# Performance work log

Measured on AMD Instinct MI355X. Metric: run time of the kernel, lower is better.

## Reference

```python
import jax, jax.numpy as jnp
import numpy as np

EPS = 1e-3  # keras BatchNormalization default epsilon


def _dwconv_t(y, w):
    # depthwise conv along time (axis 1), SAME padding. y:(B,T,S,G,n), w:(G,n,k)
    k = w.shape[-1]
    T = y.shape[1]
    pl = (k - 1) // 2
    yp = jnp.pad(y, ((0, 0), (pl, k - 1 - pl), (0, 0), (0, 0), (0, 0)))
    return sum(yp[:, j:j + T] * w[..., j] for j in range(k))


def _tc_layer(x, w, b, k3, k5, k7, gamma, beta, mu, var):
    # x:(B,T,S,C); w:(5,G,Cg,nb); b/gamma/beta/mu/var:(5,G,nb); k*:(G,nb,k)
    B, T, S, C = x.shape
    G, nb = w.shape[1], w.shape[-1]
    # global spatial pooling: concat [x, max, mean] along spatial axis -> S+2
    x = jnp.concatenate([x, x.max(axis=2, keepdims=True), x.mean(axis=2, keepdims=True)], axis=2)
    S = S + 2
    xg = x.reshape(B, T, S, G, C // G)
    # 5 grouped 1x1x1 pointwise convs at once
    y = jnp.einsum('btsgc,pgcn->pbtsgn', xg, w) + b[:, None, None, None]
    t0 = y[0]
    t3 = _dwconv_t(y[1], k3)
    t5 = _dwconv_t(y[2], k5)
    t7 = _dwconv_t(y[3], k7)
    # temporal maxpool pool=2 stride=1 SAME (TF pads right)
    t1 = jnp.maximum(y[4], jnp.concatenate([y[4][:, 1:], y[4][:, -1:]], axis=1))
    ts = jnp.stack([t0, t3, t5, t7, t1])  # (5,B,T,S,G,nb)
    scale = gamma[:, None, None, None] / jnp.sqrt(var[:, None, None, None] + EPS)
    ts = (ts - mu[:, None, None, None]) * scale + beta[:, None, None, None]
    # concat branches within each group: (B,T,S,G,5*nb)
    z = jnp.transpose(ts, (1, 2, 3, 4, 0, 5)).reshape(B, T, S, G, 5 * nb)
    z = jax.nn.relu(z)
    # channel shuffle: (G, per) -> (per, G) -> flatten
    z = jnp.swapaxes(z, -1, -2).reshape(B, T, S, G * 5 * nb)
    # MaxPooling3D pool=(2,1,1) stride 2 valid: halve T
    return jnp.maximum(z[:, 0::2], z[:, 1::2])


def setup_inputs() -> dict:
    key = jax.random.key(0)
    ks = jax.random.split(key, 32)
    B, T, H, W, C = 16, 64, 7, 7, 1024
    G = 8
    d = {'x': jax.random.normal(ks[0], (B, T, H, W, C), jnp.float32)}
    specs = [(0, 128, 32), (1, 160, 40)]  # (layer, Cg, nb)
    i = 1
    for l, cg, nb in specs:
        d[f'w{l}'] = 0.02 * jax.random.normal(ks[i], (5, G, cg, nb)); i += 1
        d[f'b{l}'] = 0.02 * jax.random.normal(ks[i], (5, G, nb)); i += 1
        d[f'k3_{l}'] = 0.1 * jax.random.normal(ks[i], (G, nb, 3)); i += 1
        d[f'k5_{l}'] = 0.1 * jax.random.normal(ks[i], (G, nb, 5)); i += 1
        d[f'k7_{l}'] = 0.1 * jax.random.normal(ks[i], (G, nb, 7)); i += 1
        d[f'g{l}'] = jax.random.uniform(ks[i], (5, G, nb), minval=0.5, maxval=1.5); i += 1
        d[f'be{l}'] = 0.02 * jax.random.normal(ks[i], (5, G, nb)); i += 1
        d[f'mu{l}'] = 0.02 * jax.random.normal(ks[i], (5, G, nb)); i += 1
        d[f'v{l}'] = jax.random.uniform(ks[i], (5, G, nb), minval=0.5, maxval=1.5); i += 1
    return d


def reference(x, w0, b0, k3_0, k5_0, k7_0, g0, be0, mu0, v0,
              w1, b1, k3_1, k5_1, k7_1, g1, be1, mu1, v1):
    B, T, H, W, C = x.shape
    z = x.reshape(B, T, H * W, C)  # (B,T,S,C), side_dim2=1 kept implicit
    z = _tc_layer(z, w0, b0, k3_0, k5_0, k7_0, g0, be0, mu0, v0)
    z = _tc_layer(z, w1, b1, k3_1, k5_1, k7_1, g1, be1, mu1, v1)
    return z[:, :, :, None, :]  # (B, T/4, S+4, 1, Cout)
```

## Files before the change

### kernel.cpp

```cpp
#include <hip/hip_runtime.h>
#include <hip/hip_bf16.h>

#define EPSBN 1e-3f

typedef __attribute__((ext_vector_type(8))) short bf16x8;
typedef __attribute__((ext_vector_type(8))) unsigned short ushort8;
typedef __attribute__((ext_vector_type(4))) float f32x4;


__device__ __forceinline__ float bf2f(unsigned short u) {
    union { unsigned int i; float f; } c; c.i = (unsigned int)u << 16; return c.f;
}
__device__ __forceinline__ unsigned short f2bf(float f) {
    union { float f; unsigned int i; } c; c.f = f;
    unsigned int r = c.i + 0x7FFF + ((c.i >> 16) & 1);
    return (unsigned short)(r >> 16);
}

__global__ __launch_bounds__(256) void tc_prep(const float* __restrict__ w0,
                                               const float* __restrict__ w1,
                                               unsigned short* __restrict__ W0t,
                                               unsigned short* __restrict__ W1t) {
    const int idx = blockIdx.x * 256 + threadIdx.x;
    if (idx < 163840) {
        const int g   = idx / 20480;
        const int rem = idx - g*20480;
        const int n   = rem >> 7;
        const int k   = rem & 127;
        const int p   = n >> 5, nn = n & 31;
        W0t[idx] = f2bf(w0[(((size_t)p*8 + g)*128 + k)*32 + nn]);
    } else if (idx < 163840 + 256000) {
        const int i2  = idx - 163840;
        const int g   = i2 / 32000;
        const int rem = i2 - g*32000;
        const int n   = rem / 160;
        const int k   = rem - n*160;
        const int kref = (k % 20)*8 + k/20;
        const int p   = n / 40, nn = n - p*40;
        W1t[i2] = f2bf(w1[(((size_t)p*8 + g)*160 + kref)*40 + nn]);
    }
}

__global__ __launch_bounds__(256) void tc_reduce0(const float* __restrict__ x,
                                                  unsigned short* __restrict__ xb,
                                                  unsigned short* __restrict__ extb,
                                                  const int big) {
    const int bt = blockIdx.x;
    const int b  = bt >> 6, t = bt & 63;
    const int c  = threadIdx.x * 4;
    const float4* src = reinterpret_cast<const float4*>(x + (size_t)bt * 49 * 1024 + c);
    float4 v = src[0];
    float mx0 = v.x, mx1 = v.y, mx2 = v.z, mx3 = v.w;
    float sm0 = v.x, sm1 = v.y, sm2 = v.z, sm3 = v.w;
    if (big) {
        ushort4 o; o.x=f2bf(v.x); o.y=f2bf(v.y); o.z=f2bf(v.z); o.w=f2bf(v.w);
        *reinterpret_cast<ushort4*>(&xb[((size_t)(b*51)*64 + t)*1024 + c]) = o;
    }
    for (int s = 1; s < 49; ++s) {
        float4 u = src[(size_t)s * 256];
        mx0 = fmaxf(mx0, u.x); sm0 += u.x;
        mx1 = fmaxf(mx1, u.y); sm1 += u.y;
        mx2 = fmaxf(mx2, u.z); sm2 += u.z;
        mx3 = fmaxf(mx3, u.w); sm3 += u.w;
        if (big) {
            ushort4 o; o.x=f2bf(u.x); o.y=f2bf(u.y); o.z=f2bf(u.z); o.w=f2bf(u.w);
            *reinterpret_cast<ushort4*>(&xb[((size_t)(b*51 + s)*64 + t)*1024 + c]) = o;
        }
    }
    const float inv = 1.0f / 49.0f;
    ushort4 omx, omn;
    omx.x=f2bf(mx0); omx.y=f2bf(mx1); omx.z=f2bf(mx2); omx.w=f2bf(mx3);
    omn.x=f2bf(sm0*inv); omn.y=f2bf(sm1*inv); omn.z=f2bf(sm2*inv); omn.w=f2bf(sm3*inv);
    if (big) {
        *reinterpret_cast<ushort4*>(&xb[((size_t)(b*51 + 49)*64 + t)*1024 + c]) = omx;
        *reinterpret_cast<ushort4*>(&xb[((size_t)(b*51 + 50)*64 + t)*1024 + c]) = omn;
    } else {
        *reinterpret_cast<ushort4*>(&extb[((size_t)(b*2 + 0)*64 + t)*1024 + c]) = omx;
        *reinterpret_cast<ushort4*>(&extb[((size_t)(b*2 + 1)*64 + t)*1024 + c]) = omn;
    }
}

template<int BIG>
__global__ __launch_bounds__(256, 5) void tc_layer0(
    const float* __restrict__ x, const unsigned short* __restrict__ xb,
    const unsigned short* __restrict__ extb,
    const unsigned short* __restrict__ W0t, const float* __restrict__ bias,
    const float* __restrict__ k3, const float* __restrict__ k5,
    const float* __restrict__ k7,
    const float* __restrict__ gam, const float* __restrict__ bet,
    const float* __restrict__ mu, const float* __restrict__ var,
    unsigned short* __restrict__ zb)
{
    const int tid = threadIdx.x;
    const int g  = blockIdx.x / 816;
    const int bs = blockIdx.x % 816;
    const int s  = bs % 51;
    const int b  = bs / 51;

    __shared__ __align__(16) unsigned short lds[15104];
    unsigned short* AtU = lds;
    unsigned short* WtU = lds + 64*136;
    unsigned short* Ytb = lds;

    #pragma unroll
    for (int it = 0; it < 4; ++it) {
        const int fid = tid + it*256;
        const int row = fid >> 4;
        const int ch8 = (fid & 15) * 8;
        ushort8 u;
        if (BIG) {
            u = *reinterpret_cast<const ushort8*>(
                &xb[((size_t)(b*51 + s)*64 + row)*1024 + g*128 + ch8]);
        } else if (s < 49) {
            const float* sp = x + ((size_t)(b*64 + row)*49 + s)*1024 + g*128 + ch8;
            const float4 f0 = *reinterpret_cast<const float4*>(sp);
            const float4 f1 = *reinterpret_cast<const float4*>(sp + 4);
            u[0]=f2bf(f0.x); u[1]=f2bf(f0.y); u[2]=f2bf(f0.z); u[3]=f2bf(f0.w);
            u[4]=f2bf(f1.x); u[5]=f2bf(f1.y); u[6]=f2bf(f1.z); u[7]=f2bf(f1.w);
        } else {
            u = *reinterpret_cast<const ushort8*>(
                &extb[((size_t)(b*2 + (s-49))*64 + row)*1024 + g*128 + ch8]);
        }
        *reinterpret_cast<ushort8*>(&AtU[row*136 + ch8]) = u;
    }

    const int lane = tid & 63;
    const int wid  = tid >> 6;
    const int fr   = lane & 15;
    const int kb   = lane >> 4;

    f32x4 zero = {0.f, 0.f, 0.f, 0.f};
    f32x4 acc[10];
    #pragma unroll
    for (int i = 0; i < 10; ++i) acc[i] = zero;

    for (int kc = 0; kc < 4; ++kc) {
        __syncthreads();
        #pragma unroll
        for (int it = 0; it < 3; ++it) {
            const int gi = tid + it*256;
            if (gi < 640) {
                const int n = gi >> 2, part = (gi & 3) * 8;
                *reinterpret_cast<ushort8*>(&WtU[n*40 + part]) =
                    *reinterpret_cast<const ushort8*>(
                        &W0t[((size_t)g*160 + n)*128 + kc*32 + part]);
            }
        }
        __syncthreads();
        const bf16x8 bfrag = *reinterpret_cast<const bf16x8*>(
            &AtU[(wid*16 + fr)*136 + kc*32 + kb*8]);
        #pragma unroll
        for (int nt = 0; nt < 10; ++nt) {
            const bf16x8 afrag = *reinterpret_cast<const bf16x8*>(
                &WtU[(nt*16 + fr)*40 + kb*8]);
            acc[nt] = __builtin_amdgcn_mfma_f32_16x16x32_bf16(afrag, bfrag, acc[nt], 0, 0, 0);
        }
    }
    __syncthreads();
    #pragma unroll
    for (int nt = 0; nt < 10; ++nt)
        #pragma unroll
        for (int r = 0; r < 4; ++r)
            Ytb[(nt*16 + kb*4 + r)*70 + wid*16 + fr] = f2bf(acc[nt][r]);
    __syncthreads();

    if (tid < 160) {
        const int ch = tid;
        const int p  = ch >> 5, n = ch & 31;
        const int pi = (p*8 + g)*32 + n;
        const float bsv = bias[pi];
        const float sc  = gam[pi]*rsqrtf(var[pi]+EPSBN);
        const float sh  = bet[pi] - mu[pi]*sc;
        float yv[64];
        #pragma unroll
        for (int i = 0; i < 32; ++i) {
            const unsigned int w2 = *reinterpret_cast<const unsigned int*>(&Ytb[ch*70 + i*2]);
            yv[2*i]   = bf2f((unsigned short)(w2 & 0xffffu)) + bsv;
            yv[2*i+1] = bf2f((unsigned short)(w2 >> 16)) + bsv;
        }
        unsigned short* zp = zb + ((size_t)(b*32)*53 + s)*1280 + g*160 + ch;
        if (p == 0) {
            #pragma unroll
            for (int tq = 0; tq < 32; ++tq) {
                const float r = fmaxf(fmaxf(fmaf(yv[2*tq],sc,sh), fmaf(yv[2*tq+1],sc,sh)), 0.f);
                zp[(size_t)tq*67840] = f2bf(r);
            }
        } else if (p == 1) {
            const float w0_ = k3[(g*32+n)*3+0], w1_ = k3[(g*32+n)*3+1], w2_ = k3[(g*32+n)*3+2];
            #pragma unroll
            for (int tq = 0; tq < 32; ++tq) {
                float a = yv[2*tq]*w1_;
                if (tq > 0) a = fmaf(yv[2*tq-1], w0_, a);
                a = fmaf(yv[2*tq+1], w2_, a);
                float c2 = fmaf(yv[2*tq], w0_, yv[2*tq+1]*w1_);
                if (tq < 31) c2 = fmaf(yv[2*tq+2], w2_, c2);
                const float r = fmaxf(fmaxf(fmaf(a,sc,sh), fmaf(c2,sc,sh)), 0.f);
                zp[(size_t)tq*67840] = f2bf(r);
            }
        } else if (p == 2) {
            float wk[5];
            #pragma unroll
            for (int j = 0; j < 5; ++j) wk[j] = k5[(g*32+n)*5+j];
            #pragma unroll
            for (int tq = 0; tq < 32; ++tq) {
                float vv[2];
                #pragma unroll
                for (int q = 0; q < 2; ++q) {
                    const int t = 2*tq + q;
                    float v = 0.f;
                    #pragma unroll
                    for (int j = 0; j < 5; ++j) {
                        const int ttp = t + j - 2;
                        if (ttp >= 0 && ttp < 64) v = fmaf(yv[ttp], wk[j], v);
                    }
                    vv[q] = v;
                }
                const float r = fmaxf(fmaxf(fmaf(vv[0],sc,sh), fmaf(vv[1],sc,sh)), 0.f);
                zp[(size_t)tq*67840] = f2bf(r);
            }
        } else if (p == 3) {
            float wk[7];
            #pragma unroll
            for (int j = 0; j < 7; ++j) wk[j] = k7[(g*32+n)*7+j];
            #pragma unroll
            for (int tq = 0; tq < 32; ++tq) {
                float vv[2];
                #pragma unroll
                for (int q = 0; q < 2; ++q) {
                    const int t = 2*tq + q;
                    float v = 0.f;
                    #pragma unroll
                    for (int j = 0; j < 7; ++j) {
                        const int ttp = t + j - 3;
                        if (ttp >= 0 && ttp < 64) v = fmaf(yv[ttp], wk[j], v);
                    }
                    vv[q] = v;
                }
                const float r = fmaxf(fmaxf(fmaf(vv[0],sc,sh), fmaf(vv[1],sc,sh)), 0.f);
                zp[(size_t)tq*67840] = f2bf(r);
            }
        } else {
            #pragma unroll
            for (int tq = 0; tq < 32; ++tq) {
                const float v0 = fmaxf(yv[2*tq], yv[2*tq+1]);
                const float v1 = fmaxf(yv[2*tq+1], yv[(2*tq+2 < 64) ? 2*tq+2 : 63]);
                const float r = fmaxf(fmaxf(fmaf(v0,sc,sh), fmaf(v1,sc,sh)), 0.f);
                zp[(size_t)tq*67840] = f2bf(r);
            }
        }
    }
}

__global__ __launch_bounds__(320) void tc_reduce1(unsigned short* __restrict__ zb) {
    const int bt = blockIdx.x;
    const int c  = threadIdx.x * 4;
    unsigned short* base = zb + (size_t)bt * 67840;
    ushort4 u = *reinterpret_cast<const ushort4*>(&base[c]);
    float v0 = bf2f(u.x), v1 = bf2f(u.y), v2 = bf2f(u.z), v3 = bf2f(u.w);
    float mx0 = v0, mx1 = v1, mx2 = v2, mx3 = v3;
    float sm0 = v0, sm1 = v1, sm2 = v2, sm3 = v3;
    for (int s = 1; s < 51; ++s) {
        ushort4 w = *reinterpret_cast<const ushort4*>(&base[(size_t)s*1280 + c]);
        v0 = bf2f(w.x); v1 = bf2f(w.y); v2 = bf2f(w.z); v3 = bf2f(w.w);
        mx0 = fmaxf(mx0, v0); sm0 += v0;
        mx1 = fmaxf(mx1, v1); sm1 += v1;
        mx2 = fmaxf(mx2, v2); sm2 += v2;
        mx3 = fmaxf(mx3, v3); sm3 += v3;
    }
    const float inv = 1.0f / 51.0f;
    ushort4 o;
    o.x = f2bf(mx0); o.y = f2bf(mx1); o.z = f2bf(mx2); o.w = f2bf(mx3);
    *reinterpret_cast<ushort4*>(&base[(size_t)51*1280 + c]) = o;
    o.x = f2bf(sm0*inv); o.y = f2bf(sm1*inv); o.z = f2bf(sm2*inv); o.w = f2bf(sm3*inv);
    *reinterpret_cast<ushort4*>(&base[(size_t)52*1280 + c]) = o;
}

__global__ __launch_bounds__(256, 4) void tc_layer1(
    const unsigned short* __restrict__ zbi,
    const unsigned short* __restrict__ W1t, const float* __restrict__ bias,
    const float* __restrict__ k3, const float* __restrict__ k5,
    const float* __restrict__ k7,
    const float* __restrict__ gam, const float* __restrict__ bet,
    const float* __restrict__ mu, const float* __restrict__ var,
    unsigned short* __restrict__ og)
{
    const int tid = threadIdx.x;
    const int g   = blockIdx.x / 432;
    const int rem = blockIdx.x % 432;
    const int sp  = rem % 27;
    const int b   = rem / 27;
    const int s0  = sp*2;
    const int has1 = (s0 + 1 < 53);

    __shared__ __align__(16) unsigned short lds[64*168 + 208*40];
    unsigned short* AtU = lds;
    unsigned short* WtU = lds + 64*168;
    unsigned short* Ytb = lds;

    if (tid < 40) {
        ushort8 z8 = {0,0,0,0,0,0,0,0};
        const int r = tid / 5, cp = tid - r*5;
        *reinterpret_cast<ushort8*>(&WtU[(200 + r)*40 + cp*8]) = z8;
    }

    #pragma unroll
    for (int it = 0; it < 10; ++it) {
        const int fid = tid + it*256;
        const int row = fid / 40;
        const int seg = fid - row*40;
        const int gg  = seg / 5, q = seg - gg*5;
        const int ch  = gg*160 + g*20 + q*4;
        const int s   = (row < 32) ? s0 : (has1 ? s0+1 : s0);
        const int t   = row & 31;
        const unsigned short* src = zbi + ((size_t)(b*32 + t)*53 + s)*1280 + ch;
        *reinterpret_cast<ushort4*>(&AtU[row*168 + seg*4]) =
            *reinterpret_cast<const ushort4*>(src);
    }

    const int lane = tid & 63;
    const int wid  = tid >> 6;
    const int fr   = lane & 15;
    const int kb   = lane >> 4;

    f32x4 zero = {0.f, 0.f, 0.f, 0.f};
    f32x4 acc[13];
    #pragma unroll
    for (int i = 0; i < 13; ++i) acc[i] = zero;

    for (int kc = 0; kc < 5; ++kc) {
        __syncthreads();
        #pragma unroll
        for (int it = 0; it < 4; ++it) {
            const int gi = tid + it*256;
            if (gi < 800) {
                const int n = gi >> 2, part = (gi & 3) * 8;
                *reinterpret_cast<ushort8*>(&WtU[n*40 + part]) =
                    *reinterpret_cast<const ushort8*>(
                        &W1t[((size_t)g*200 + n)*160 + kc*32 + part]);
            }
        }
        __syncthreads();
        const bf16x8 bfrag = *reinterpret_cast<const bf16x8*>(
            &AtU[(wid*16 + fr)*168 + kc*32 + kb*8]);
        #pragma unroll
        for (int nt = 0; nt < 13; ++nt) {
            const bf16x8 afrag = *reinterpret_cast<const bf16x8*>(
                &WtU[(nt*16 + fr)*40 + kb*8]);
            acc[nt] = __builtin_amdgcn_mfma_f32_16x16x32_bf16(afrag, bfrag, acc[nt], 0, 0, 0);
        }
    }
    __syncthreads();
    #pragma unroll
    for (int nt = 0; nt < 13; ++nt) {
        #pragma unroll
        for (int r = 0; r < 4; ++r) {
            const int n = nt*16 + kb*4 + r;
            if (n < 200) Ytb[n*70 + wid*16 + fr] = f2bf(acc[nt][r]);
        }
    }
    __syncthreads();

    #pragma unroll
    for (int it = 0; it < 2; ++it) {
        const int task = tid + it*256;
        if (task < 400) {
            const int sIdx = (task >= 200) ? 1 : 0;
            const int ch   = task - sIdx*200;
            if (sIdx && !has1) continue;
            const int s  = s0 + sIdx;
            const int p  = ch / 40, n = ch - p*40;
            const int pi = (p*8 + g)*40 + n;
            const float bsv = bias[pi];
            const float sc  = gam[pi]*rsqrtf(var[pi]+EPSBN);
            const float sh  = bet[pi] - mu[pi]*sc;
            float yv[32];
            #pragma unroll
            for (int i = 0; i < 16; ++i) {
                const unsigned int w2 = *reinterpret_cast<const unsigned int*>(
                    &Ytb[ch*70 + sIdx*32 + i*2]);
                yv[2*i]   = bf2f((unsigned short)(w2 & 0xffffu)) + bsv;
                yv[2*i+1] = bf2f((unsigned short)(w2 >> 16)) + bsv;
            }
            unsigned short* op = og + ((size_t)(b*16)*53 + s)*1600 + g*200 + ch;
            if (p == 0) {
                #pragma unroll
                for (int tq = 0; tq < 16; ++tq) {
                    const float r = fmaxf(fmaxf(fmaf(yv[2*tq],sc,sh), fmaf(yv[2*tq+1],sc,sh)), 0.f);
                    op[(size_t)tq*84800] = f2bf(r);
                }
            } else if (p == 1) {
                const float w0_ = k3[(g*40+n)*3+0], w1_ = k3[(g*40+n)*3+1], w2_ = k3[(g*40+n)*3+2];
                #pragma unroll
                for (int tq = 0; tq < 16; ++tq) {
                    float a = yv[2*tq]*w1_;
                    if (tq > 0) a = fmaf(yv[2*tq-1], w0_, a);
                    a = fmaf(yv[2*tq+1], w2_, a);
                    float c2 = fmaf(yv[2*tq], w0_, yv[2*tq+1]*w1_);
                    if (tq < 15) c2 = fmaf(yv[2*tq+2], w2_, c2);
                    const float r = fmaxf(fmaxf(fmaf(a,sc,sh), fmaf(c2,sc,sh)), 0.f);
                    op[(size_t)tq*84800] = f2bf(r);
                }
            } else if (p == 2) {
                float wk[5];
                #pragma unroll
                for (int j = 0; j < 5; ++j) wk[j] = k5[(g*40+n)*5+j];
                #pragma unroll
                for (int tq = 0; tq < 16; ++tq) {
                    float vv[2];
                    #pragma unroll
                    for (int q = 0; q < 2; ++q) {
                        const int t = 2*tq + q;
                        float v = 0.f;
                        #pragma unroll
                        for (int j = 0; j < 5; ++j) {
                            const int ttp = t + j - 2;
                            if (ttp >= 0 && ttp < 32) v = fmaf(yv[ttp], wk[j], v);
                        }
                        vv[q] = v;
                    }
                    const float r = fmaxf(fmaxf(fmaf(vv[0],sc,sh), fmaf(vv[1],sc,sh)), 0.f);
                    op[(size_t)tq*84800] = f2bf(r);
                }
            } else if (p == 3) {
                float wk[7];
                #pragma unroll
                for (int j = 0; j < 7; ++j) wk[j] = k7[(g*40+n)*7+j];
                #pragma unroll
                for (int tq = 0; tq < 16; ++tq) {
                    float vv[2];
                    #pragma unroll
                    for (int q = 0; q < 2; ++q) {
                        const int t = 2*tq + q;
                        float v = 0.f;
                        #pragma unroll
                        for (int j = 0; j < 7; ++j) {
                            const int ttp = t + j - 3;
                            if (ttp >= 0 && ttp < 32) v = fmaf(yv[ttp], wk[j], v);
                        }
                        vv[q] = v;
                    }
                    const float r = fmaxf(fmaxf(fmaf(vv[0],sc,sh), fmaf(vv[1],sc,sh)), 0.f);
                    op[(size_t)tq*84800] = f2bf(r);
                }
            } else {
                #pragma unroll
                for (int tq = 0; tq < 16; ++tq) {
                    const float v0 = fmaxf(yv[2*tq], yv[2*tq+1]);
                    const float v1 = fmaxf(yv[2*tq+1], yv[(2*tq+2 < 32) ? 2*tq+2 : 31]);
                    const float r = fmaxf(fmaxf(fmaf(v0,sc,sh), fmaf(v1,sc,sh)), 0.f);
                    op[(size_t)tq*84800] = f2bf(r);
                }
            }
        }
    }
}

__global__ __launch_bounds__(256) void tc_shuffle(const unsigned short* __restrict__ og,
                                                  float* __restrict__ o) {
    __shared__ unsigned short row[1600];
    const size_t base = (size_t)blockIdx.x * 1600;
    const int tid = threadIdx.x;
    if (tid < 200)
        *reinterpret_cast<ushort8*>(&row[tid*8]) =
            *reinterpret_cast<const ushort8*>(&og[base + (size_t)tid*8]);
    __syncthreads();
    #pragma unroll
    for (int it = 0; it < 2; ++it) {
        const int f4 = tid + it*256;
        if (f4 < 400) {
            const int c = f4*4;
            float4 v;
            v.x = bf2f(row[((c  ) & 7)*200 + ((c  ) >> 3)]);
            v.y = bf2f(row[((c+1) & 7)*200 + ((c+1) >> 3)]);
            v.z = bf2f(row[((c+2) & 7)*200 + ((c+2) >> 3)]);
            v.w = bf2f(row[((c+3) & 7)*200 + ((c+3) >> 3)]);
            *reinterpret_cast<float4*>(&o[base + (size_t)c]) = v;
        }
    }
}

extern "C" void kernel_launch(void* const* d_in, const int* in_sizes, int n_in,
                              void* d_out, int out_size, void* d_ws, size_t ws_size,
                              hipStream_t stream) {
    const float* x    = (const float*)d_in[0];
    const float* w0   = (const float*)d_in[1];
    const float* b0   = (const float*)d_in[2];
    const float* k3_0 = (const float*)d_in[3];
    const float* k5_0 = (const float*)d_in[4];
    const float* k7_0 = (const float*)d_in[5];
    const float* g0   = (const float*)d_in[6];
    const float* be0  = (const float*)d_in[7];
    const float* mu0  = (const float*)d_in[8];
    const float* v0   = (const float*)d_in[9];
    const float* w1   = (const float*)d_in[10];
    const float* b1   = (const float*)d_in[11];
    const float* k3_1 = (const float*)d_in[12];
    const float* k5_1 = (const float*)d_in[13];
    const float* k7_1 = (const float*)d_in[14];
    const float* g1   = (const float*)d_in[15];
    const float* be1  = (const float*)d_in[16];
    const float* mu1  = (const float*)d_in[17];
    const float* v1   = (const float*)d_in[18];

    const size_t n_zb   = 34734080;
    const size_t n_W0t  = 163840;
    const size_t n_W1t  = 256000;
    const size_t n_extb = 2097152;
    const size_t n_og   = 21708800;
    const size_t n_xb   = 53477376;

    unsigned short* zb   = (unsigned short*)d_ws;
    unsigned short* W0t  = zb + n_zb;
    unsigned short* W1t  = W0t + n_W0t;
    unsigned short* extb = W1t + n_W1t;
    unsigned short* og   = extb + n_extb;
    unsigned short* xb   = og + n_og;
    const size_t need_big = (n_zb + n_W0t + n_W1t + n_extb + n_og + n_xb) * 2;
    const int big = (ws_size >= need_big) ? 1 : 0;

    tc_prep   <<<1640, 256, 0, stream>>>(w0, w1, W0t, W1t);
    tc_reduce0<<<16*64, 256, 0, stream>>>(x, xb, extb, big);
    if (big)
        tc_layer0<1><<<816*8, 256, 0, stream>>>(x, xb, extb, W0t, b0, k3_0, k5_0,
                                                k7_0, g0, be0, mu0, v0, zb);
    else
        tc_layer0<0><<<816*8, 256, 0, stream>>>(x, xb, extb, W0t, b0, k3_0, k5_0,
                                                k7_0, g0, be0, mu0, v0, zb);
    tc_reduce1<<<16*32, 320, 0, stream>>>(zb);
    tc_layer1 <<<432*8, 256, 0, stream>>>(zb, W1t, b1, k3_1, k5_1, k7_1,
                                          g1, be1, mu1, v1, og);
    tc_shuffle<<<16*16*53, 256, 0, stream>>>(og, (float*)d_out);
}
```

Baseline: 265.1 us.

## Process two spatial positions per layer0 block to reuse loaded weight tiles

Each tc_layer0 block now handles two spatial positions (128 time rows) with 512 threads instead of one position with 256. The weight tile staged in LDS per k-chunk is shared by 8 waves instead of 4, halving weight reloads and block count. The epilogue splits 320 threads across both positions, guarding the odd final position. This costs more LDS per block and may reduce occupancy, and the last block redundantly loads a duplicate position.

```diff
diff --git a/kernel.cpp b/kernel.cpp
--- a/kernel.cpp
+++ b/kernel.cpp
@@ -81,7 +81,7 @@
 }
 
 template<int BIG>
-__global__ __launch_bounds__(256, 5) void tc_layer0(
+__global__ __launch_bounds__(512, 6) void tc_layer0(
     const float* __restrict__ x, const unsigned short* __restrict__ xb,
     const unsigned short* __restrict__ extb,
     const unsigned short* __restrict__ W0t, const float* __restrict__ bias,
@@ -92,34 +92,38 @@
     unsigned short* __restrict__ zb)
 {
     const int tid = threadIdx.x;
-    const int g  = blockIdx.x / 816;
-    const int bs = blockIdx.x % 816;
-    const int s  = bs % 51;
-    const int b  = bs / 51;
-
-    __shared__ __align__(16) unsigned short lds[15104];
+    const int g   = blockIdx.x / 416;
+    const int rem = blockIdx.x % 416;
+    const int sp  = rem % 26;
+    const int b   = rem / 26;
+    const int s0  = sp*2;
+    const int has1 = (s0 + 1 < 51);
+
+    __shared__ __align__(16) unsigned short lds[128*136 + 160*40];
     unsigned short* AtU = lds;
-    unsigned short* WtU = lds + 64*136;
+    unsigned short* WtU = lds + 128*136;
     unsigned short* Ytb = lds;
 
     #pragma unroll
     for (int it = 0; it < 4; ++it) {
-        const int fid = tid + it*256;
+        const int fid = tid + it*512;
         const int row = fid >> 4;
         const int ch8 = (fid & 15) * 8;
+        const int t   = row & 63;
+        const int s   = (row < 64) ? s0 : (has1 ? s0+1 : s0);
         ushort8 u;
         if (BIG) {
             u = *reinterpret_cast<const ushort8*>(
-                &xb[((size_t)(b*51 + s)*64 + row)*1024 + g*128 + ch8]);
+                &xb[((size_t)(b*51 + s)*64 + t)*1024 + g*128 + ch8]);
         } else if (s < 49) {
-            const float* sp = x + ((size_t)(b*64 + row)*49 + s)*1024 + g*128 + ch8;
-            const float4 f0 = *reinterpret_cast<const float4*>(sp);
-            const float4 f1 = *reinterpret_cast<const float4*>(sp + 4);
+            const float* sp_ = x + ((size_t)(b*64 + t)*49 + s)*1024 + g*128 + ch8;
+            const float4 f0 = *reinterpret_cast<const float4*>(sp_);
+            const float4 f1 = *reinterpret_cast<const float4*>(sp_ + 4);
             u[0]=f2bf(f0.x); u[1]=f2bf(f0.y); u[2]=f2bf(f0.z); u[3]=f2bf(f0.w);
             u[4]=f2bf(f1.x); u[5]=f2bf(f1.y); u[6]=f2bf(f1.z); u[7]=f2bf(f1.w);
         } else {
             u = *reinterpret_cast<const ushort8*>(
-                &extb[((size_t)(b*2 + (s-49))*64 + row)*1024 + g*128 + ch8]);
+                &extb[((size_t)(b*2 + (s-49))*64 + t)*1024 + g*128 + ch8]);
         }
         *reinterpret_cast<ushort8*>(&AtU[row*136 + ch8]) = u;
     }
@@ -137,8 +141,8 @@
     for (int kc = 0; kc < 4; ++kc) {
         __syncthreads();
         #pragma unroll
-        for (int it = 0; it < 3; ++it) {
-            const int gi = tid + it*256;
+        for (int it = 0; it < 2; ++it) {
+            const int gi = tid + it*512;
             if (gi < 640) {
                 const int n = gi >> 2, part = (gi & 3) * 8;
                 *reinterpret_cast<ushort8*>(&WtU[n*40 + part]) =
@@ -161,91 +165,96 @@
     for (int nt = 0; nt < 10; ++nt)
         #pragma unroll
         for (int r = 0; r < 4; ++r)
-            Ytb[(nt*16 + kb*4 + r)*70 + wid*16 + fr] = f2bf(acc[nt][r]);
+            Ytb[(nt*16 + kb*4 + r)*134 + wid*16 + fr] = f2bf(acc[nt][r]);
     __syncthreads();
 
-    if (tid < 160) {
-        const int ch = tid;
-        const int p  = ch >> 5, n = ch & 31;
-        const int pi = (p*8 + g)*32 + n;
-        const float bsv = bias[pi];
-        const float sc  = gam[pi]*rsqrtf(var[pi]+EPSBN);
-        const float sh  = bet[pi] - mu[pi]*sc;
-        float yv[64];
-        #pragma unroll
-        for (int i = 0; i < 32; ++i) {
-            const unsigned int w2 = *reinterpret_cast<const unsigned int*>(&Ytb[ch*70 + i*2]);
-            yv[2*i]   = bf2f((unsigned short)(w2 & 0xffffu)) + bsv;
-            yv[2*i+1] = bf2f((unsigned short)(w2 >> 16)) + bsv;
-        }
-        unsigned short* zp = zb + ((size_t)(b*32)*53 + s)*1280 + g*160 + ch;
-        if (p == 0) {
+    if (tid < 320) {
+        const int sIdx = (tid >= 160) ? 1 : 0;
+        const int ch   = tid - sIdx*160;
+        if (!sIdx || has1) {
+            const int s  = s0 + sIdx;
+            const int p  = ch >> 5, n = ch & 31;
+            const int pi = (p*8 + g)*32 + n;
+            const float bsv = bias[pi];
+            const float sc  = gam[pi]*rsqrtf(var[pi]+EPSBN);
+            const float sh  = bet[pi] - mu[pi]*sc;
+            float yv[64];
             #pragma unroll
-            for (int tq = 0; tq < 32; ++tq) {
-                const float r = fmaxf(fmaxf(fmaf(yv[2*tq],sc,sh), fmaf(yv[2*tq+1],sc,sh)), 0.f);
-                zp[(size_t)tq*67840] = f2bf(r);
+            for (int i = 0; i < 32; ++i) {
+                const unsigned int w2 = *reinterpret_cast<const unsigned int*>(
+                    &Ytb[ch*134 + sIdx*64 + i*2]);
+                yv[2*i]   = bf2f((unsigned short)(w2 & 0xffffu)) + bsv;
+                yv[2*i+1] = bf2f((unsigned short)(w2 >> 16)) + bsv;
             }
-        } else if (p == 1) {
-            const float w0_ = k3[(g*32+n)*3+0], w1_ = k3[(g*32+n)*3+1], w2_ = k3[(g*32+n)*3+2];
-            #pragma unroll
-            for (int tq = 0; tq < 32; ++tq) {
-                float a = yv[2*tq]*w1_;
-                if (tq > 0) a = fmaf(yv[2*tq-1], w0_, a);
-                a = fmaf(yv[2*tq+1], w2_, a);
-                float c2 = fmaf(yv[2*tq], w0_, yv[2*tq+1]*w1_);
-                if (tq < 31) c2 = fmaf(yv[2*tq+2], w2_, c2);
-                const float r = fmaxf(fmaxf(fmaf(a,sc,sh), fmaf(c2,sc,sh)), 0.f);
-                zp[(size_t)tq*67840] = f2bf(r);
-            }
-        } else if (p == 2) {
-            float wk[5];
-            #pragma unroll
-            for (int j = 0; j < 5; ++j) wk[j] = k5[(g*32+n)*5+j];
-            #pragma unroll
-            for (int tq = 0; tq < 32; ++tq) {
-                float vv[2];
-                #pragma unroll
-                for (int q = 0; q < 2; ++q) {
-                    const int t = 2*tq + q;
-                    float v = 0.f;
+            unsigned short* zp = zb + ((size_t)(b*32)*53 + s)*1280 + g*160 + ch;
+            if (p == 0) {
+                #pragma unroll
+                for (int tq = 0; tq < 32; ++tq) {
+                    const float r = fmaxf(fmaxf(fmaf(yv[2*tq],sc,sh), fmaf(yv[2*tq+1],sc,sh)), 0.f);
+                    zp[(size_t)tq*67840] = f2bf(r);
+                }
+            } else if (p == 1) {
+                const float w0_ = k3[(g*32+n)*3+0], w1_ = k3[(g*32+n)*3+1], w2_ = k3[(g*32+n)*3+2];
+                #pragma unroll
+                for (int tq = 0; tq < 32; ++tq) {
+                    float a = yv[2*tq]*w1_;
+                    if (tq > 0) a = fmaf(yv[2*tq-1], w0_, a);
+                    a = fmaf(yv[2*tq+1], w2_, a);
+                    float c2 = fmaf(yv[2*tq], w0_, yv[2*tq+1]*w1_);
+                    if (tq < 31) c2 = fmaf(yv[2*tq+2], w2_, c2);
+                    const float r = fmaxf(fmaxf(fmaf(a,sc,sh), fmaf(c2,sc,sh)), 0.f);
+                    zp[(size_t)tq*67840] = f2bf(r);
+                }
+            } else if (p == 2) {
+                float wk[5];
+                #pragma unroll
+                for (int j = 0; j < 5; ++j) wk[j] = k5[(g*32+n)*5+j];
+                #pragma unroll
+                for (int tq = 0; tq < 32; ++tq) {
+                    float vv[2];
                     #pragma unroll
-                    for (int j = 0; j < 5; ++j) {
-                        const int ttp = t + j - 2;
-                        if (ttp >= 0 && ttp < 64) v = fmaf(yv[ttp], wk[j], v);
+                    for (int q = 0; q < 2; ++q) {
+                        const int t = 2*tq + q;
+                        float v = 0.f;
+                        #pragma unroll
+                        for (int j = 0; j < 5; ++j) {
+                            const int ttp = t + j - 2;
+                            if (ttp >= 0 && ttp < 64) v = fmaf(yv[ttp], wk[j], v);
+                        }
+                        vv[q] = v;
                     }
-                    vv[q] = v;
-                }
-                const float r = fmaxf(fmaxf(fmaf(vv[0],sc,sh), fmaf(vv[1],sc,sh)), 0.f);
-                zp[(size_t)tq*67840] = f2bf(r);
-            }
-        } else if (p == 3) {
-            float wk[7];
-            #pragma unroll
-            for (int j = 0; j < 7; ++j) wk[j] = k7[(g*32+n)*7+j];
-            #pragma unroll
-            for (int tq = 0; tq < 32; ++tq) {
-                float vv[2];
-                #pragma unroll
-                for (int q = 0; q < 2; ++q) {
-                    const int t = 2*tq + q;
-                    float v = 0.f;
+                    const float r = fmaxf(fmaxf(fmaf(vv[0],sc,sh), fmaf(vv[1],sc,sh)), 0.f);
+                    zp[(size_t)tq*67840] = f2bf(r);
+                }
+            } else if (p == 3) {
+                float wk[7];
+                #pragma unroll
+                for (int j = 0; j < 7; ++j) wk[j] = k7[(g*32+n)*7+j];
+                #pragma unroll
+                for (int tq = 0; tq < 32; ++tq) {
+                    float vv[2];
                     #pragma unroll
-                    for (int j = 0; j < 7; ++j) {
-                        const int ttp = t + j - 3;
-                        if (ttp >= 0 && ttp < 64) v = fmaf(yv[ttp], wk[j], v);
+                    for (int q = 0; q < 2; ++q) {
+                        const int t = 2*tq + q;
+                        float v = 0.f;
+                        #pragma unroll
+                        for (int j = 0; j < 7; ++j) {
+                            const int ttp = t + j - 3;
+                            if (ttp >= 0 && ttp < 64) v = fmaf(yv[ttp], wk[j], v);
+                        }
+                        vv[q] = v;
                     }
-                    vv[q] = v;
-                }
-                const float r = fmaxf(fmaxf(fmaf(vv[0],sc,sh), fmaf(vv[1],sc,sh)), 0.f);
-                zp[(size_t)tq*67840] = f2bf(r);
-            }
-        } else {
-            #pragma unroll
-            for (int tq = 0; tq < 32; ++tq) {
-                const float v0 = fmaxf(yv[2*tq], yv[2*tq+1]);
-                const float v1 = fmaxf(yv[2*tq+1], yv[(2*tq+2 < 64) ? 2*tq+2 : 63]);
-                const float r = fmaxf(fmaxf(fmaf(v0,sc,sh), fmaf(v1,sc,sh)), 0.f);
-                zp[(size_t)tq*67840] = f2bf(r);
+                    const float r = fmaxf(fmaxf(fmaf(vv[0],sc,sh), fmaf(vv[1],sc,sh)), 0.f);
+                    zp[(size_t)tq*67840] = f2bf(r);
+                }
+            } else {
+                #pragma unroll
+                for (int tq = 0; tq < 32; ++tq) {
+                    const float v0 = fmaxf(yv[2*tq], yv[2*tq+1]);
+                    const float v1 = fmaxf(yv[2*tq+1], yv[(2*tq+2 < 64) ? 2*tq+2 : 63]);
+                    const float r = fmaxf(fmaxf(fmaf(v0,sc,sh), fmaf(v1,sc,sh)), 0.f);
+                    zp[(size_t)tq*67840] = f2bf(r);
+                }
             }
         }
     }
@@ -521,10 +530,10 @@
     tc_prep   <<<1640, 256, 0, stream>>>(w0, w1, W0t, W1t);
     tc_reduce0<<<16*64, 256, 0, stream>>>(x, xb, extb, big);
     if (big)
-        tc_layer0<1><<<816*8, 256, 0, stream>>>(x, xb, extb, W0t, b0, k3_0, k5_0,
+        tc_layer0<1><<<416*8, 512, 0, stream>>>(x, xb, extb, W0t, b0, k3_0, k5_0,
                                                 k7_0, g0, be0, mu0, v0, zb);
     else
-        tc_layer0<0><<<816*8, 256, 0, stream>>>(x, xb, extb, W0t, b0, k3_0, k5_0,
+        tc_layer0<0><<<416*8, 512, 0, stream>>>(x, xb, extb, W0t, b0, k3_0, k5_0,
                                                 k7_0, g0, be0, mu0, v0, zb);
     tc_reduce1<<<16*32, 320, 0, stream>>>(zb);
     tc_layer1 <<<432*8, 256, 0, stream>>>(zb, W1t, b1, k3_1, k5_1, k7_1,
```

Result: no change. 266.3 us (+0.5%).
